# Kernel optimization log

Measured on AMD Instinct MI355X. Metric: run time of the kernel, lower is better.

The kernel has to match this reference:

```python
import jax, jax.numpy as jnp
import numpy as np

# FlowNetC correlation config: kernel_size=1, so no kernel-window averaging;
# pad_size == max_displacement -> output spatial size == input spatial size.
B, C, H, W = 8, 256, 48, 64
MAX_DISP = 20   # max_displacement
STRIDE2 = 2     # displacement stride
PAD = 20        # pad_size
GRID_RAD = MAX_DISP // STRIDE2            # 10
GRID_W = 2 * GRID_RAD + 1                 # 21 -> 441 displacement channels


def setup_inputs() -> dict:
    key = jax.random.key(0)
    k1, k2 = jax.random.split(key)
    return {
        "input1": jax.random.normal(k1, (B, C, H, W), dtype=jnp.float32),
        "input2": jax.random.normal(k2, (B, C, H, W), dtype=jnp.float32),
    }


def _correlation(input1, input2):
    b, c, h, w = input1.shape
    p2 = jnp.pad(input2, ((0, 0), (0, 0), (PAD, PAD), (PAD, PAD)))
    # Displacement start offsets into the padded map. dy-major ordering matches
    # the CUDA kernel: top_channel = dy_idx * GRID_W + dx_idx.
    d = np.arange(-GRID_RAD, GRID_RAD + 1) * STRIDE2 + PAD  # [21]
    offs = np.stack(np.meshgrid(d, d, indexing="ij"), axis=-1).reshape(-1, 2)
    offs = jnp.asarray(offs, dtype=jnp.int32)  # [441, 2] (dy, dx)
    sumelems = jnp.float32(c)  # kernel_size^2 * C with kernel_size=1

    def step(carry, o):
        shifted = jax.lax.dynamic_slice(p2, (0, 0, o[0], o[1]), (b, c, h, w))
        # mean over channels of elementwise product -> [B, H, W]
        return carry, jnp.sum(input1 * shifted, axis=1) / sumelems

    _, ys = jax.lax.scan(step, 0, offs)          # [441, B, H, W]
    return jnp.transpose(ys, (1, 0, 2, 3))       # [B, 441, H, W]


def reference(input1, input2):
    return _correlation(input1, input2)
```

## Files before the change

### kernel.cpp

```cpp
#include <hip/hip_runtime.h>

typedef __bf16 bf16x8 __attribute__((ext_vector_type(8)));
typedef float f32x4 __attribute__((ext_vector_type(4)));
typedef float f32x16 __attribute__((ext_vector_type(16)));

#define CC 256
#define HH 48
#define WW 64
#define HW (HH * WW)
#define NB 8
#define GW 21

__global__ __launch_bounds__(256) void prep_kernel(const float* __restrict__ in1,
                                                   const float* __restrict__ in2,
                                                   unsigned short* __restrict__ o1,
                                                   unsigned short* __restrict__ o2)
{
    __shared__ float lds[CC * 33];
    int blk  = blockIdx.x;
    int sel  = (blk >= 768);
    int blk2 = sel ? blk - 768 : blk;
    int b  = blk2 & 7;
    int st = blk2 >> 3;
    int s0 = st * 32;
    const float* src = sel ? in2 : in1;
    unsigned short* dst = sel ? o2 : o1;
    float scale = sel ? 1.0f : (1.0f / 256.0f);

    int t = threadIdx.x;
    int sidx  = t & 31;
    int cbase = t >> 5;
    const float* sb = src + (size_t)b * CC * HW + s0;
    #pragma unroll
    for (int p = 0; p < 32; ++p) {
        int c = cbase + p * 8;
        lds[c * 33 + sidx] = sb[(size_t)c * HW + sidx] * scale;
    }
    __syncthreads();

    int y  = s0 >> 6;
    int xb = s0 & 63;
    int s  = t & 31;
    int c8 = t >> 5;
    unsigned short* db = dst + (size_t)(b * HH + y) * 32 * 64 * 8;
    int x = xb + s;
    int xoff = (x & 1) * 32 + (x >> 1);
    #pragma unroll
    for (int it = 0; it < 4; ++it) {
        int cblk = it * 8 + c8;
        unsigned dw[4];
        #pragma unroll
        for (int d = 0; d < 4; ++d) {
            unsigned u0 = __builtin_bit_cast(unsigned, lds[(cblk * 8 + 2 * d) * 33 + s]);
            u0 += 0x7fffu + ((u0 >> 16) & 1u);
            unsigned u1 = __builtin_bit_cast(unsigned, lds[(cblk * 8 + 2 * d + 1) * 33 + s]);
            u1 += 0x7fffu + ((u1 >> 16) & 1u);
            dw[d] = (u0 >> 16) | (u1 & 0xffff0000u);
        }
        *(uint4*)(db + ((size_t)cblk * 64 + xoff) * 8) =
            make_uint4(dw[0], dw[1], dw[2], dw[3]);
    }
}

__global__ __launch_bounds__(256, 4) void corr_kernel(const unsigned short* __restrict__ in1F,
                                                      const unsigned short* __restrict__ in2F,
                                                      float* __restrict__ out)
{
    __shared__ unsigned char smem[36864];
    unsigned short* Bl = (unsigned short*)smem;

    int blk  = blockIdx.x;
    int b    = blk & 7;
    int t2   = blk >> 3;
    int ysrc = t2 / 6 - 20;
    int jg   = t2 - (t2 / 6) * 6;
    int tid  = threadIdx.x;
    int w    = tid >> 6;
    int lane = tid & 63;

    int j  = 6 * w + jg;
    int yo = ysrc - 2 * (j - 10);
    bool jvalid = (j <= 20) && (yo >= 0) && (yo < HH);

    float* orow = jvalid
        ? out + (((size_t)(b * 441 + j * GW)) * HH + yo) * WW
        : out;

    if (ysrc < 0 || ysrc >= HH) {
        if (jvalid) {
            #pragma unroll
            for (int jx = 0; jx < GW; ++jx)
                __builtin_nontemporal_store(0.0f, orow + (size_t)jx * HW + lane);
        }
        return;
    }

    int l31 = lane & 31;
    int q2  = lane >> 5;

    const unsigned short* arow = jvalid
        ? in1F + ((size_t)(b * HH + yo) * 32 + q2) * 512 + (size_t)l31 * 8
        : in1F;

    bf16x8 Ab[4][2], Bb[2][2];
    if (jvalid) {
        #pragma unroll
        for (int kr = 0; kr < 3; ++kr)
            #pragma unroll
            for (int p = 0; p < 2; ++p)
                Ab[kr][p] = *(const bf16x8*)(arow + (size_t)kr * 1024 + p * 256);
    }

    {
        const unsigned short* bsrc = in2F + (size_t)(b * HH + ysrc) * (32 * 64 * 8);
        #pragma unroll
        for (int it = 0; it < 8; ++it) {
            size_t off = ((size_t)it * 256 + tid) * 8;
            *(uint4*)(Bl + off) = *(const uint4*)(bsrc + off);
        }
    }
    __syncthreads();

    f32x16 acc[2];
    if (jvalid) {
        const unsigned short* brow = Bl + (size_t)q2 * 512 + (size_t)l31 * 8;

        acc[0] = (f32x16)(0.0f);
        acc[1] = (f32x16)(0.0f);

        #pragma unroll
        for (int p = 0; p < 2; ++p)
            Bb[0][p] = *(const bf16x8*)(brow + p * 256);

        #pragma unroll
        for (int kk = 0; kk < 16; ++kk) {
            if (kk < 13) {
                #pragma unroll
                for (int p = 0; p < 2; ++p)
                    Ab[(kk + 3) & 3][p] =
                        *(const bf16x8*)(arow + (size_t)(kk + 3) * 1024 + p * 256);
            }
            if (kk < 15) {
                #pragma unroll
                for (int p = 0; p < 2; ++p)
                    Bb[(kk + 1) & 1][p] =
                        *(const bf16x8*)(brow + (size_t)(kk + 1) * 1024 + p * 256);
            }
            #pragma unroll
            for (int p = 0; p < 2; ++p)
                acc[p] = __builtin_amdgcn_mfma_f32_32x32x16_bf16(
                    Ab[kk & 3][p], Bb[kk & 1][p], acc[p], 0, 0, 0);
        }
    }

    __syncthreads();

    if (!jvalid) return;

    float* dtw = (float*)smem + w * 2304;
    #pragma unroll
    for (int p = 0; p < 2; ++p) {
        #pragma unroll
        for (int rq = 0; rq < 4; ++rq) {
            f32x4 v = { acc[p][4 * rq], acc[p][4 * rq + 1],
                        acc[p][4 * rq + 2], acc[p][4 * rq + 3] };
            *(f32x4*)(dtw + (size_t)(p * 32 + l31) * 36 + rq * 8 + q2 * 4) = v;
        }
    }

    int xe = lane >> 1;
    int pp = lane & 1;
    #pragma unroll
    for (int jx = 0; jx < GW; ++jx) {
        int ce = xe + jx - 10;
        float v = (ce >= 0 && ce < 32) ? dtw[(size_t)(pp * 32 + ce) * 36 + xe] : 0.0f;
        __builtin_nontemporal_store(v, orow + (size_t)jx * HW + lane);
    }
}

extern "C" void kernel_launch(void* const* d_in, const int* in_sizes, int n_in,
                              void* d_out, int out_size, void* d_ws, size_t ws_size,
                              hipStream_t stream)
{
    (void)in_sizes; (void)n_in; (void)out_size; (void)ws_size;
    const float* in1 = (const float*)d_in[0];
    const float* in2 = (const float*)d_in[1];
    float* out = (float*)d_out;

    unsigned short* in1F = (unsigned short*)d_ws;
    unsigned short* in2F = in1F + (size_t)NB * HW * CC;

    prep_kernel<<<dim3(1536), dim3(256), 0, stream>>>(in1, in2, in1F, in2F);
    corr_kernel<<<dim3(NB * 88 * 6), dim3(256), 0, stream>>>(in1F, in2F, out);
}
```

Before: 116.3 us.

## Restructure correlation blocks to keep input1 rows in registers and stream input2 rows

After: 150.4 us. 29.3% more time.

```diff
diff --git a/kernel.cpp b/kernel.cpp
--- a/kernel.cpp
+++ b/kernel.cpp
@@ -62,119 +62,116 @@
     }
 }
 
-__global__ __launch_bounds__(256, 4) void corr_kernel(const unsigned short* __restrict__ in1F,
+__global__ __launch_bounds__(384, 3) void corr_kernel(const unsigned short* __restrict__ in1F,
                                                       const unsigned short* __restrict__ in2F,
                                                       float* __restrict__ out)
 {
-    __shared__ unsigned char smem[36864];
+    __shared__ unsigned char smem[60416];
     unsigned short* Bl = (unsigned short*)smem;
+    float* dtall = (float*)(smem + 32768);
 
-    int blk  = blockIdx.x;
-    int b    = blk & 7;
-    int t2   = blk >> 3;
-    int ysrc = t2 / 6 - 20;
-    int jg   = t2 - (t2 / 6) * 6;
+    int blk = blockIdx.x;
+    int b   = blk & 7;
+    int r   = blk >> 3;
+    int g   = r & 15;
+    int dh  = r >> 4;
+    int yo0 = (g >> 1) * 6 + (g & 1);
+    int d0  = (dh == 0) ? 0 : (5 * dh + 1);
+    int PD  = (dh == 0) ? 6 : 5;
+    int NT  = PD + 2;
+
     int tid  = threadIdx.x;
     int w    = tid >> 6;
     int lane = tid & 63;
+    int p    = w & 1;
+    int a    = w >> 1;
+    int yo   = yo0 + 2 * a;
+    int l31  = lane & 31;
+    int q2   = lane >> 5;
 
-    int j  = 6 * w + jg;
-    int yo = ysrc - 2 * (j - 10);
-    bool jvalid = (j <= 20) && (yo >= 0) && (yo < HH);
+    const unsigned short* arow = in1F + (size_t)(b * HH + yo) * 16384
+                               + q2 * 512 + p * 256 + l31 * 8;
+    bf16x8 Ar[16];
+    #pragma unroll
+    for (int kk = 0; kk < 16; ++kk)
+        Ar[kk] = *(const bf16x8*)(arow + kk * 1024);
 
-    float* orow = jvalid
-        ? out + (((size_t)(b * 441 + j * GW)) * HH + yo) * WW
-        : out;
+    int ysrc0 = yo0 + 2 * d0 - 20;
 
-    if (ysrc < 0 || ysrc >= HH) {
-        if (jvalid) {
+    uint4 sreg[6];
+    {
+        int ys = ysrc0;
+        if (ys >= 0 && ys < HH) {
+            const uint4* srcp = (const uint4*)(in2F + (size_t)(b * HH + ys) * 16384);
             #pragma unroll
-            for (int jx = 0; jx < GW; ++jx)
-                __builtin_nontemporal_store(0.0f, orow + (size_t)jx * HW + lane);
-        }
-        return;
-    }
-
-    int l31 = lane & 31;
-    int q2  = lane >> 5;
-
-    const unsigned short* arow = jvalid
-        ? in1F + ((size_t)(b * HH + yo) * 32 + q2) * 512 + (size_t)l31 * 8
-        : in1F;
-
-    bf16x8 Ab[4][2], Bb[2][2];
-    if (jvalid) {
-        #pragma unroll
-        for (int kr = 0; kr < 3; ++kr)
-            #pragma unroll
-            for (int p = 0; p < 2; ++p)
-                Ab[kr][p] = *(const bf16x8*)(arow + (size_t)kr * 1024 + p * 256);
-    }
-
-    {
-        const unsigned short* bsrc = in2F + (size_t)(b * HH + ysrc) * (32 * 64 * 8);
-        #pragma unroll
-        for (int it = 0; it < 8; ++it) {
-            size_t off = ((size_t)it * 256 + tid) * 8;
-            *(uint4*)(Bl + off) = *(const uint4*)(bsrc + off);
-        }
-    }
-    __syncthreads();
-
-    f32x16 acc[2];
-    if (jvalid) {
-        const unsigned short* brow = Bl + (size_t)q2 * 512 + (size_t)l31 * 8;
-
-        acc[0] = (f32x16)(0.0f);
-        acc[1] = (f32x16)(0.0f);
-
-        #pragma unroll
-        for (int p = 0; p < 2; ++p)
-            Bb[0][p] = *(const bf16x8*)(brow + p * 256);
-
-        #pragma unroll
-        for (int kk = 0; kk < 16; ++kk) {
-            if (kk < 13) {
-                #pragma unroll
-                for (int p = 0; p < 2; ++p)
-                    Ab[(kk + 3) & 3][p] =
-                        *(const bf16x8*)(arow + (size_t)(kk + 3) * 1024 + p * 256);
-            }
-            if (kk < 15) {
-                #pragma unroll
-                for (int p = 0; p < 2; ++p)
-                    Bb[(kk + 1) & 1][p] =
-                        *(const bf16x8*)(brow + (size_t)(kk + 1) * 1024 + p * 256);
-            }
-            #pragma unroll
-            for (int p = 0; p < 2; ++p)
-                acc[p] = __builtin_amdgcn_mfma_f32_32x32x16_bf16(
-                    Ab[kk & 3][p], Bb[kk & 1][p], acc[p], 0, 0, 0);
+            for (int i = 0; i < 6; ++i)
+                if (i < 5 || tid < 128) sreg[i] = srcp[i * 384 + tid];
         }
     }
 
-    __syncthreads();
+    float* dta = dtall + a * 2304;
+    const unsigned short* bfr = Bl + q2 * 512 + p * 256 + l31 * 8;
+    int xe = lane >> 1;
+    int pe = lane & 1;
 
-    if (!jvalid) return;
+    for (int t = 0; t < NT; ++t) {
+        int ys  = ysrc0 + 2 * t;
+        bool vs = (ys >= 0 && ys < HH);
 
-    float* dtw = (float*)smem + w * 2304;
-    #pragma unroll
-    for (int p = 0; p < 2; ++p) {
-        #pragma unroll
-        for (int rq = 0; rq < 4; ++rq) {
-            f32x4 v = { acc[p][4 * rq], acc[p][4 * rq + 1],
-                        acc[p][4 * rq + 2], acc[p][4 * rq + 3] };
-            *(f32x4*)(dtw + (size_t)(p * 32 + l31) * 36 + rq * 8 + q2 * 4) = v;
+        __syncthreads();
+        if (vs) {
+            uint4* dst = (uint4*)Bl;
+            #pragma unroll
+            for (int i = 0; i < 6; ++i)
+                if (i < 5 || tid < 128) dst[i * 384 + tid] = sreg[i];
         }
-    }
+        __syncthreads();
 
-    int xe = lane >> 1;
-    int pp = lane & 1;
-    #pragma unroll
-    for (int jx = 0; jx < GW; ++jx) {
-        int ce = xe + jx - 10;
-        float v = (ce >= 0 && ce < 32) ? dtw[(size_t)(pp * 32 + ce) * 36 + xe] : 0.0f;
-        __builtin_nontemporal_store(v, orow + (size_t)jx * HW + lane);
+        if (t + 1 < NT) {
+            int ys2 = ys + 2;
+            if (ys2 >= 0 && ys2 < HH) {
+                const uint4* srcp = (const uint4*)(in2F + (size_t)(b * HH + ys2) * 16384);
+                #pragma unroll
+                for (int i = 0; i < 6; ++i)
+                    if (i < 5 || tid < 128) sreg[i] = srcp[i * 384 + tid];
+            }
+        }
+
+        int ta   = t - a;
+        bool act = (ta >= 0) && (ta < PD);
+
+        if (act && vs) {
+            f32x16 acc = (f32x16)(0.0f);
+            bf16x8 Bb[2];
+            Bb[0] = *(const bf16x8*)bfr;
+            #pragma unroll
+            for (int kk = 0; kk < 16; ++kk) {
+                if (kk < 15)
+                    Bb[(kk + 1) & 1] = *(const bf16x8*)(bfr + (kk + 1) * 1024);
+                acc = __builtin_amdgcn_mfma_f32_32x32x16_bf16(Ar[kk], Bb[kk & 1], acc, 0, 0, 0);
+            }
+            #pragma unroll
+            for (int rq = 0; rq < 4; ++rq) {
+                f32x4 v = { acc[4 * rq], acc[4 * rq + 1],
+                            acc[4 * rq + 2], acc[4 * rq + 3] };
+                *(f32x4*)(dta + p * 1152 + l31 * 36 + rq * 8 + q2 * 4) = v;
+            }
+        }
+        __syncthreads();
+
+        if (act) {
+            int dy = d0 + ta;
+            float* obase = out + (((size_t)(b * 441 + dy * GW)) * HH + yo) * WW;
+            #pragma unroll
+            for (int jj = 0; jj < 11; ++jj) {
+                int jx = 2 * jj + p;
+                if (jx > 20) continue;
+                int ce = xe + jx - 10;
+                float v = (vs && ce >= 0 && ce < 32)
+                        ? dta[pe * 1152 + ce * 36 + xe] : 0.0f;
+                __builtin_nontemporal_store(v, obase + (size_t)jx * HW + lane);
+            }
+        }
     }
 }
 
@@ -191,5 +188,5 @@
     unsigned short* in2F = in1F + (size_t)NB * HW * CC;
 
     prep_kernel<<<dim3(1536), dim3(256), 0, stream>>>(in1, in2, in1F, in2F);
-    corr_kernel<<<dim3(NB * 88 * 6), dim3(256), 0, stream>>>(in1F, in2F, out);
+    corr_kernel<<<dim3(512), dim3(384), 0, stream>>>(in1F, in2F, out);
 }
```

## Process two source rows per block to reuse input1 A-fragments across displacements

Applied to the files above, without the earlier changes.

New measurement: 117.5 us. About the same (+1.0%).

```diff
diff --git a/kernel.cpp b/kernel.cpp
--- a/kernel.cpp
+++ b/kernel.cpp
@@ -62,35 +62,45 @@
     }
 }
 
-__global__ __launch_bounds__(256, 4) void corr_kernel(const unsigned short* __restrict__ in1F,
+__global__ __launch_bounds__(256, 2) void corr_kernel(const unsigned short* __restrict__ in1F,
                                                       const unsigned short* __restrict__ in2F,
                                                       float* __restrict__ out)
 {
-    __shared__ unsigned char smem[36864];
+    __shared__ unsigned char smem[65536];
     unsigned short* Bl = (unsigned short*)smem;
 
-    int blk  = blockIdx.x;
-    int b    = blk & 7;
-    int t2   = blk >> 3;
-    int ysrc = t2 / 6 - 20;
-    int jg   = t2 - (t2 / 6) * 6;
+    int blk = blockIdx.x;
+    int b   = blk & 7;
+    int r   = blk >> 3;
+    int yi  = r / 3;
+    int jg  = r - yi * 3;
+    int ys0 = yi - 20;
+    int ys1 = ys0 + 2;
+
     int tid  = threadIdx.x;
     int w    = tid >> 6;
     int lane = tid & 63;
-
-    int j  = 6 * w + jg;
-    int yo = ysrc - 2 * (j - 10);
-    bool jvalid = (j <= 20) && (yo >= 0) && (yo < HH);
-
-    float* orow = jvalid
-        ? out + (((size_t)(b * 441 + j * GW)) * HH + yo) * WW
-        : out;
-
-    if (ysrc < 0 || ysrc >= HH) {
-        if (jvalid) {
+    int q    = jg * 4 + w;
+    int yo   = ys0 + 20 - 4 * q;
+    int j0   = 2 * q;
+    bool v1  = (q <= 9);
+    bool wvalid = (q <= 10) && (yo >= 0) && (yo < HH);
+    bool vs0 = (ys0 >= 0) && (ys0 < HH);
+    bool vs1 = (ys1 >= 0) && (ys1 < HH);
+
+    float* orow0 = out + (((size_t)(b * 441 + j0 * GW)) * HH + yo) * WW;
+    float* orow1 = orow0 + (size_t)GW * HW;
+
+    if (!vs0 && !vs1) {
+        if (wvalid) {
             #pragma unroll
             for (int jx = 0; jx < GW; ++jx)
-                __builtin_nontemporal_store(0.0f, orow + (size_t)jx * HW + lane);
+                __builtin_nontemporal_store(0.0f, orow0 + (size_t)jx * HW + lane);
+            if (v1) {
+                #pragma unroll
+                for (int jx = 0; jx < GW; ++jx)
+                    __builtin_nontemporal_store(0.0f, orow1 + (size_t)jx * HW + lane);
+            }
         }
         return;
     }
@@ -98,12 +108,11 @@
     int l31 = lane & 31;
     int q2  = lane >> 5;
 
-    const unsigned short* arow = jvalid
-        ? in1F + ((size_t)(b * HH + yo) * 32 + q2) * 512 + (size_t)l31 * 8
-        : in1F;
-
-    bf16x8 Ab[4][2], Bb[2][2];
-    if (jvalid) {
+    const unsigned short* arow = in1F
+        + ((size_t)(b * HH + (wvalid ? yo : 0)) * 32 + q2) * 512 + (size_t)l31 * 8;
+
+    bf16x8 Ab[4][2], Bb[2][2][2];
+    if (wvalid) {
         #pragma unroll
         for (int kr = 0; kr < 3; ++kr)
             #pragma unroll
@@ -112,25 +121,35 @@
     }
 
     {
-        const unsigned short* bsrc = in2F + (size_t)(b * HH + ysrc) * (32 * 64 * 8);
-        #pragma unroll
-        for (int it = 0; it < 8; ++it) {
-            size_t off = ((size_t)it * 256 + tid) * 8;
-            *(uint4*)(Bl + off) = *(const uint4*)(bsrc + off);
+        uint4* dst = (uint4*)Bl;
+        if (vs0) {
+            const uint4* s = (const uint4*)(in2F + (size_t)(b * HH + ys0) * 16384);
+            #pragma unroll
+            for (int i = 0; i < 8; ++i) dst[i * 256 + tid] = s[i * 256 + tid];
+        }
+        if (vs1) {
+            const uint4* s = (const uint4*)(in2F + (size_t)(b * HH + ys1) * 16384);
+            #pragma unroll
+            for (int i = 0; i < 8; ++i) dst[2048 + i * 256 + tid] = s[i * 256 + tid];
         }
     }
     __syncthreads();
 
-    f32x16 acc[2];
-    if (jvalid) {
-        const unsigned short* brow = Bl + (size_t)q2 * 512 + (size_t)l31 * 8;
-
-        acc[0] = (f32x16)(0.0f);
-        acc[1] = (f32x16)(0.0f);
-
-        #pragma unroll
-        for (int p = 0; p < 2; ++p)
-            Bb[0][p] = *(const bf16x8*)(brow + p * 256);
+    f32x16 acc[2][2];
+    if (wvalid) {
+        const unsigned short* brow = Bl + q2 * 512 + (size_t)l31 * 8;
+
+        #pragma unroll
+        for (int jj = 0; jj < 2; ++jj)
+            #pragma unroll
+            for (int p = 0; p < 2; ++p)
+                acc[jj][p] = (f32x16)(0.0f);
+
+        #pragma unroll
+        for (int jj = 0; jj < 2; ++jj)
+            #pragma unroll
+            for (int p = 0; p < 2; ++p)
+                Bb[0][jj][p] = *(const bf16x8*)(brow + jj * 16384 + p * 256);
 
         #pragma unroll
         for (int kk = 0; kk < 16; ++kk) {
@@ -142,39 +161,47 @@
             }
             if (kk < 15) {
                 #pragma unroll
+                for (int jj = 0; jj < 2; ++jj)
+                    #pragma unroll
+                    for (int p = 0; p < 2; ++p)
+                        Bb[(kk + 1) & 1][jj][p] =
+                            *(const bf16x8*)(brow + jj * 16384 + (size_t)(kk + 1) * 1024 + p * 256);
+            }
+            #pragma unroll
+            for (int jj = 0; jj < 2; ++jj)
+                #pragma unroll
                 for (int p = 0; p < 2; ++p)
-                    Bb[(kk + 1) & 1][p] =
-                        *(const bf16x8*)(brow + (size_t)(kk + 1) * 1024 + p * 256);
-            }
-            #pragma unroll
-            for (int p = 0; p < 2; ++p)
-                acc[p] = __builtin_amdgcn_mfma_f32_32x32x16_bf16(
-                    Ab[kk & 3][p], Bb[kk & 1][p], acc[p], 0, 0, 0);
+                    acc[jj][p] = __builtin_amdgcn_mfma_f32_32x32x16_bf16(
+                        Ab[kk & 3][p], Bb[kk & 1][jj][p], acc[jj][p], 0, 0, 0);
         }
     }
 
     __syncthreads();
-
-    if (!jvalid) return;
+    if (!wvalid) return;
 
     float* dtw = (float*)smem + w * 2304;
+    int xe = lane >> 1;
+    int pe = lane & 1;
     #pragma unroll
-    for (int p = 0; p < 2; ++p) {
-        #pragma unroll
-        for (int rq = 0; rq < 4; ++rq) {
-            f32x4 v = { acc[p][4 * rq], acc[p][4 * rq + 1],
-                        acc[p][4 * rq + 2], acc[p][4 * rq + 3] };
-            *(f32x4*)(dtw + (size_t)(p * 32 + l31) * 36 + rq * 8 + q2 * 4) = v;
-        }
-    }
-
-    int xe = lane >> 1;
-    int pp = lane & 1;
-    #pragma unroll
-    for (int jx = 0; jx < GW; ++jx) {
-        int ce = xe + jx - 10;
-        float v = (ce >= 0 && ce < 32) ? dtw[(size_t)(pp * 32 + ce) * 36 + xe] : 0.0f;
-        __builtin_nontemporal_store(v, orow + (size_t)jx * HW + lane);
+    for (int jj = 0; jj < 2; ++jj) {
+        if (jj == 1 && !v1) continue;
+        bool vsj = jj ? vs1 : vs0;
+        float* orow = jj ? orow1 : orow0;
+        #pragma unroll
+        for (int p = 0; p < 2; ++p)
+            #pragma unroll
+            for (int rq = 0; rq < 4; ++rq) {
+                f32x4 v = { acc[jj][p][4 * rq], acc[jj][p][4 * rq + 1],
+                            acc[jj][p][4 * rq + 2], acc[jj][p][4 * rq + 3] };
+                *(f32x4*)(dtw + (size_t)(p * 32 + l31) * 36 + rq * 8 + q2 * 4) = v;
+            }
+        #pragma unroll
+        for (int jx = 0; jx < GW; ++jx) {
+            int ce = xe + jx - 10;
+            float val = (vsj && ce >= 0 && ce < 32)
+                      ? dtw[(size_t)(pe * 32 + ce) * 36 + xe] : 0.0f;
+            __builtin_nontemporal_store(val, orow + (size_t)jx * HW + lane);
+        }
     }
 }
 
@@ -191,5 +218,5 @@
     unsigned short* in2F = in1F + (size_t)NB * HW * CC;
 
     prep_kernel<<<dim3(1536), dim3(256), 0, stream>>>(in1, in2, in1F, in2F);
-    corr_kernel<<<dim3(NB * 88 * 6), dim3(256), 0, stream>>>(in1F, in2F, out);
+    corr_kernel<<<dim3(NB * 88 * 3), dim3(256), 0, stream>>>(in1F, in2F, out);
 }
```
